# Kernel optimization log

Hardware: AMD Instinct MI355X
Metric: run time of the kernel (lower is better)

Reference implementation:

```python
import jax, jax.numpy as jnp
import numpy as np

NEG_SLOPE = 0.2
EPS = 1e-12


def setup_inputs() -> dict:
    key = jax.random.key(0)
    ks = jax.random.split(key, 12)
    N, IN, E, C, EF, NET = 100000, 512, 3200000, 16, 64, 8
    return {
        "head_feature": jax.random.normal(ks[0], (N, IN), jnp.float32),
        "tail_feature": jax.random.normal(ks[1], (N, IN), jnp.float32),
        "edge_index": jax.random.randint(ks[2], (2, E), 0, N, jnp.int32),
        "tmp_edge": jax.random.randint(ks[3], (E,), 0, NET, jnp.int32),
        "W": jax.random.normal(ks[4], (IN, C), jnp.float32) * 0.05,
        "W_e": jax.random.normal(ks[5], (EF, EF), jnp.float32) * 0.1,
        "a_l": jax.random.normal(ks[6], (1, 1, C), jnp.float32) * 0.3,
        "a_r": jax.random.normal(ks[7], (1, 1, C), jnp.float32) * 0.3,
        "a_e": jax.random.normal(ks[8], (1, 1, EF), jnp.float32) * 0.3,
        "edge_emb": jax.random.normal(ks[9], (NET, EF), jnp.float32) * 0.3,
        "res_W": jax.random.normal(ks[10], (IN, C), jnp.float32) * 0.05,
        "res_b": jax.random.normal(ks[11], (C,), jnp.float32) * 0.05,
    }


def reference(head_feature, tail_feature, W, W_e, a_l, a_r, a_e,
              edge_emb, res_W, res_b, edge_index, tmp_edge):
    N = head_feature.shape[0]
    H = a_l.shape[1]  # nhead = 1 in SimpleHGN_final's edge_GAT
    C = a_l.shape[2]
    head_ind, tail_ind = edge_index[0], edge_index[1]

    # projected node / edge-type features (dropout is identity in eval)
    h_head = (head_feature @ W).reshape(N, H, C)              # [N,H,C]
    h_tail = (tail_feature @ W).reshape(-1, H, C)             # [Nt,H,C]
    e = (edge_emb @ W_e).reshape(-1, H, a_e.shape[2])         # [NET,H,EF]

    # per-edge attention logits
    h_l = (a_l * h_head).sum(-1)[head_ind]                    # [E,H]
    h_r = (a_r * h_tail).sum(-1)[tail_ind]                    # [E,H]
    h_e = (a_e * e).sum(-1)[tmp_edge]                         # [E,H]
    logits = jax.nn.leaky_relu(h_l + h_r + h_e, NEG_SLOPE)    # [E,H]

    # sparse softmax over each destination (head) row, per head
    m = jax.ops.segment_max(logits, head_ind, num_segments=N)  # [N,H]
    ex = jnp.exp(logits - m[head_ind])
    denom = jax.ops.segment_sum(ex, head_ind, num_segments=N)  # [N,H]
    attn = ex / denom[head_ind]                                # [E,H]

    # SpMM aggregation: out[i] = sum_e attn[e] * h_tail[tail[e]]
    msg = attn[..., None] * h_tail[tail_ind]                   # [E,H,C]
    out = jax.ops.segment_sum(msg, head_ind, num_segments=N)   # [N,H,C]
    out = out.reshape(N, H * C)

    # node residual (nn.Linear on x_head)
    out = out + head_feature @ res_W + res_b

    # SimpleHGN_final post-processing: L2 row-normalize then softmax
    norm = jnp.linalg.norm(out, axis=1, keepdims=True)
    h_prime = out / jnp.maximum(norm, EPS)
    return jax.nn.softmax(h_prime, axis=1)
```

## Files before the change

### kernel.cpp

```cpp
#include <hip/hip_runtime.h>
#include <hip/hip_fp16.h>
#include <math.h>

#define IN_F 512
#define C_DIM 16
#define EF_DIM 64
#define BSHIFT 6
#define NPB 64
#define NBMAX2 2048
#define CNTW 2048
#define SCB 512
#define CAP 2560

typedef float f32x4 __attribute__((ext_vector_type(4)));
typedef unsigned u32x2 __attribute__((ext_vector_type(2)));
typedef _Float16 f16x8 __attribute__((ext_vector_type(8)));

union U2H { unsigned u; __half2 h; };

typedef const unsigned __attribute__((address_space(1)))* gas_u32;
typedef unsigned __attribute__((address_space(3)))* las_u32;

__device__ __forceinline__ void gld16(const float* g, float* l) {
  __builtin_amdgcn_global_load_lds((gas_u32)g, (las_u32)l, 16, 0, 0);
}

__global__ __launch_bounds__(512) void prep_kernel(
    const float* __restrict__ W, const float* __restrict__ We,
    const float* __restrict__ al, const float* __restrict__ ar,
    const float* __restrict__ ae, const float* __restrict__ emb,
    const float* __restrict__ resW, float* __restrict__ he,
    _Float16* __restrict__ Bph, _Float16* __restrict__ Bpt,
    float* __restrict__ wlt, float* __restrict__ wrt, int NET) {
  __shared__ float v[EF_DIM];
  int t = threadIdx.x;
  float wl = 0.f, wr = 0.f;
#pragma unroll
  for (int c = 0; c < C_DIM; c++) {
    float wv = W[t * C_DIM + c];
    wl += wv * al[c];
    wr += wv * ar[c];
  }
  wlt[t] = wl;
  wrt[t] = wr;
  if (t < EF_DIM) {
    float s = 0.f;
    for (int f = 0; f < EF_DIM; f++) s += We[t * EF_DIM + f] * ae[f];
    v[t] = s;
  }
  __syncthreads();
  if (t < NET) {
    float s = 0.f;
    for (int k = 0; k < EF_DIM; k++) s += emb[t * EF_DIM + k] * v[k];
    he[t] = s;
  }
  for (int i = 0; i < 16; i++) {
    int flat = t + 512 * i;
    int j = flat & 7;
    int l = (flat >> 3) & 63;
    int s = flat >> 9;
    int k = 32 * s + ((l >> 4) << 3) + j;
    int c = l & 15;
    Bph[flat] = (_Float16)resW[k * C_DIM + c];
    Bpt[flat] = (_Float16)W[k * C_DIM + c];
  }
}

__global__ __launch_bounds__(256) void proj7_kernel(
    const float* __restrict__ hf, const float* __restrict__ tf,
    const _Float16* __restrict__ Bph, const _Float16* __restrict__ Bpt,
    const float* __restrict__ wlt, const float* __restrict__ wrt,
    float* __restrict__ resid, float* __restrict__ hl,
    __half* __restrict__ ht_, float* __restrict__ hr, int N) {
  __shared__ float As[2][4096];
  int t = threadIdx.x;
  int w = __builtin_amdgcn_readfirstlane(t >> 6);
  int lane = t & 63;
  int r0 = blockIdx.x * 64;
  const float* feat = blockIdx.y ? tf : hf;
  const _Float16* Bp = blockIdx.y ? Bpt : Bph;
  const float* wv = blockIdx.y ? wrt : wlt;
  f32x4 acc0 = {0.f, 0.f, 0.f, 0.f};
  float acc1 = 0.f;
  const float* sg_src[4];
#pragma unroll
  for (int g = 0; g < 4; g++) {
    int u = (w * 4 + g) * 64 + lane;
    int r = u >> 4;
    int c = (u & 15) ^ (r & 7);
    int gr = min(r0 + r, N - 1);
    sg_src[g] = feat + (size_t)gr * IN_F + c * 4;
  }
  int row = w * 16 + (lane & 15);
  int sA[2][2];
#pragma unroll
  for (int s2 = 0; s2 < 2; s2++)
#pragma unroll
    for (int h = 0; h < 2; h++)
      sA[s2][h] = row * 16 + ((s2 * 8 + (lane >> 4) * 2 + h) ^ (row & 7));
  const float* wvp = wv + (lane >> 4) * 8;
#pragma unroll
  for (int g = 0; g < 4; g++) gld16(sg_src[g], &As[0][(w * 4 + g) * 256]);
  __syncthreads();
#pragma unroll
  for (int kc = 0; kc < 8; kc++) {
    if (kc < 7) {
      int nb = (kc + 1) & 1;
#pragma unroll
      for (int g = 0; g < 4; g++)
        gld16(sg_src[g] + (kc + 1) * 64, &As[nb][(w * 4 + g) * 256]);
    }
    const float* ab = As[kc & 1];
#pragma unroll
    for (int s2 = 0; s2 < 2; s2++) {
      f32x4 lo = *(const f32x4*)(ab + sA[s2][0] * 4);
      f32x4 hi = *(const f32x4*)(ab + sA[s2][1] * 4);
      f16x8 a = {(_Float16)lo.x, (_Float16)lo.y, (_Float16)lo.z,
                 (_Float16)lo.w, (_Float16)hi.x, (_Float16)hi.y,
                 (_Float16)hi.z, (_Float16)hi.w};
      int s = kc * 2 + s2;
      f16x8 b0 = *(const f16x8*)(Bp + (size_t)(s * 64 + lane) * 8);
      acc0 = __builtin_amdgcn_mfma_f32_16x16x32_f16(a, b0, acc0, 0, 0, 0);
      f32x4 wa = *(const f32x4*)(wvp + kc * 64 + s2 * 32);
      f32x4 wb = *(const f32x4*)(wvp + kc * 64 + s2 * 32 + 4);
      acc1 += lo.x * wa.x + lo.y * wa.y + lo.z * wa.z + lo.w * wa.w +
              hi.x * wb.x + hi.y * wb.y + hi.z * wb.z + hi.w * wb.w;
    }
    __syncthreads();
  }
  acc1 += __shfl_xor(acc1, 16, 64);
  acc1 += __shfl_xor(acc1, 32, 64);
  int col = lane & 15;
  int rb = r0 + w * 16 + (lane >> 4) * 4;
#pragma unroll
  for (int i = 0; i < 4; i++) {
    int r = rb + i;
    if (r < N) {
      if (blockIdx.y == 0)
        resid[(size_t)r * C_DIM + col] = acc0[i];
      else
        ht_[(size_t)r * C_DIM + col] = __float2half(acc0[i]);
    }
  }
  if (lane < 16) {
    int r = r0 + w * 16 + lane;
    if (r < N) {
      if (blockIdx.y == 0)
        hl[r] = acc1;
      else
        hr[r] = acc1;
    }
  }
}

__global__ __launch_bounds__(512) void hist_kernel(
    const int* __restrict__ head, unsigned* __restrict__ cnt, int E, int NB,
    int chunk) {
  __shared__ unsigned lcnt[NBMAX2];
  int tid = threadIdx.x;
  for (int b = tid; b < NB; b += 512) lcnt[b] = 0u;
  __syncthreads();
  int start = blockIdx.x * chunk;
  int end = min(E, start + chunk);
  for (int i = start + tid; i < end; i += 512)
    atomicAdd(&lcnt[((unsigned)__builtin_nontemporal_load(head + i)) >> BSHIFT],
              1u);
  __syncthreads();
  unsigned* row = cnt + (size_t)blockIdx.x * CNTW;
  for (int b = tid; b < NB; b += 512) row[b] = lcnt[b];
}

__global__ __launch_bounds__(256) void colscan_kernel(
    unsigned* __restrict__ cnt, unsigned* __restrict__ btotal, int NB) {
  int b = blockIdx.x * 256 + threadIdx.x;
  if (b >= NB) return;
  unsigned running = 0;
#pragma unroll 8
  for (int blk = 0; blk < SCB; blk++) {
    unsigned v = cnt[(size_t)blk * CNTW + b];
    cnt[(size_t)blk * CNTW + b] = running;
    running += v;
  }
  btotal[b] = running;
}

__global__ __launch_bounds__(1024) void scan_kernel(
    const unsigned* __restrict__ btotal, unsigned* __restrict__ base, int NB) {
  __shared__ unsigned ps[1024];
  int t = threadIdx.x;
  unsigned a = (2 * t < NB) ? btotal[2 * t] : 0u;
  unsigned b = (2 * t + 1 < NB) ? btotal[2 * t + 1] : 0u;
  ps[t] = a + b;
  __syncthreads();
  for (int off = 1; off < 1024; off <<= 1) {
    unsigned v = (t >= off) ? ps[t - off] : 0u;
    __syncthreads();
    ps[t] += v;
    __syncthreads();
  }
  unsigned excl = ps[t] - (a + b);
  if (2 * t < NB) base[2 * t] = excl;
  if (2 * t + 1 < NB) base[2 * t + 1] = excl + a;
  if (t == 1023) base[NB] = ps[1023];
}

__global__ __launch_bounds__(512) void scatter_kernel(
    const int* __restrict__ head, const int* __restrict__ tail,
    const int* __restrict__ ty, const unsigned* __restrict__ cnt,
    const unsigned* __restrict__ bbase, unsigned* __restrict__ rec, int E,
    int NB, int chunk) {
  __shared__ unsigned lbase[NBMAX2];
  __shared__ unsigned lcnt[NBMAX2];
  int tid = threadIdx.x;
  const unsigned* row = cnt + (size_t)blockIdx.x * CNTW;
  for (int b = tid; b < NB; b += 512) {
    lbase[b] = bbase[b] + row[b];
    lcnt[b] = 0u;
  }
  __syncthreads();
  int start = blockIdx.x * chunk;
  int end = min(E, start + chunk);
  for (int i = start + tid; i < end; i += 512) {
    unsigned h = (unsigned)__builtin_nontemporal_load(head + i);
    unsigned tl = (unsigned)__builtin_nontemporal_load(tail + i);
    unsigned t = (unsigned)__builtin_nontemporal_load(ty + i);
    unsigned b = h >> BSHIFT;
    unsigned off = atomicAdd(&lcnt[b], 1u);
    rec[lbase[b] + off] = ((h & 63u) << 20) | ((t & 7u) << 17) | tl;
  }
}

__global__ __launch_bounds__(256) void agg_kernel(
    const unsigned* __restrict__ rec, const unsigned* __restrict__ base,
    const __half* __restrict__ ht, const float* __restrict__ h_l,
    const float* __restrict__ h_r, const float* __restrict__ he_tab,
    const float* __restrict__ resid, const float* __restrict__ resb,
    float* __restrict__ out, int N, int NET) {
  __shared__ unsigned srec[CAP];
  __shared__ unsigned scnt[NPB];
  __shared__ unsigned soff[NPB + 1];
  __shared__ unsigned scur[NPB];
  __shared__ float accf[NPB * 18];
  __shared__ float hl_s[NPB];
  __shared__ float he_s[8];
  int tid = threadIdx.x;
  int b = blockIdx.x;
  int nodebase = b << BSHIFT;
  int s = (int)base[b];
  int e = (int)base[b + 1];
  int cnt_all = e - s;
  int m = min(cnt_all, CAP);
  if (tid < NPB) {
    scnt[tid] = 0u;
    int node = nodebase + tid;
    hl_s[tid] = node < N ? h_l[node] : 0.f;
  }
  if (tid < NET) he_s[tid] = he_tab[tid];
  for (int i = tid; i < NPB * 18; i += 256) accf[i] = 0.f;
  __syncthreads();
  for (int i = tid; i < m; i += 256)
    atomicAdd(&scnt[rec[(size_t)(s + i)] >> 20], 1u);
  __syncthreads();
  if (tid < NPB) {
    unsigned v = scnt[tid];
    unsigned orig = v;
    for (int off = 1; off < NPB; off <<= 1) {
      unsigned u = __shfl_up(v, off, 64);
      if (tid >= off) v += u;
    }
    soff[tid + 1] = v;
    scur[tid] = v - orig;
    if (tid == 0) soff[0] = 0u;
  }
  __syncthreads();
  for (int i = tid; i < m; i += 256) {
    unsigned r = rec[(size_t)(s + i)];
    unsigned pos = atomicAdd(&scur[r >> 20], 1u);
    srec[pos] = r;
  }
  for (int i = CAP + tid; i < cnt_all; i += 256) {
    unsigned r = rec[(size_t)(s + i)];
    int local = (int)(r >> 20);
    int typ = (int)((r >> 17) & 7u);
    int tl = (int)(r & 0x1FFFFu);
    float lg = hl_s[local] + h_r[tl] + he_s[typ];
    lg = lg > 0.f ? lg : 0.2f * lg;
    float ex = __expf(lg);
    const uint4* hp = (const uint4*)(ht + (size_t)tl * C_DIM);
    uint4 A = hp[0], B = hp[1];
    float* a = accf + local * 18;
    U2H cv;
    float2 f;
    unsigned wvv[8] = {A.x, A.y, A.z, A.w, B.x, B.y, B.z, B.w};
#pragma unroll
    for (int q = 0; q < 8; q++) {
      cv.u = wvv[q];
      f = __half22float2(cv.h);
      atomicAdd(a + 2 * q, ex * f.x);
      atomicAdd(a + 2 * q + 1, ex * f.y);
    }
    atomicAdd(a + 16, ex);
  }
  __syncthreads();
  int w = tid >> 6;
  int lane = tid & 63;
  int node_l = w * 16 + (lane >> 2);
  int p = lane & 3;
  float a[17];
#pragma unroll
  for (int k = 0; k < 17; k++) a[k] = 0.f;
  int st = (int)soff[node_l];
  int en = (int)soff[node_l + 1];
  float hlv = hl_s[node_l];
  for (int i = st + p; i < en; i += 4) {
    unsigned r = srec[i];
    int typ = (int)((r >> 17) & 7u);
    int tl = (int)(r & 0x1FFFFu);
    float lg = hlv + h_r[tl] + he_s[typ];
    lg = lg > 0.f ? lg : 0.2f * lg;
    float ex = __expf(lg);
    const uint4* hp = (const uint4*)(ht + (size_t)tl * C_DIM);
    uint4 A = hp[0], B = hp[1];
    U2H cv;
    float2 f;
    unsigned wd[8] = {A.x, A.y, A.z, A.w, B.x, B.y, B.z, B.w};
#pragma unroll
    for (int q = 0; q < 8; q++) {
      cv.u = wd[q];
      f = __half22float2(cv.h);
      a[2 * q] += ex * f.x;
      a[2 * q + 1] += ex * f.y;
    }
    a[16] += ex;
  }
#pragma unroll
  for (int k = 0; k < 17; k++) {
    a[k] += __shfl_xor(a[k], 1, 64);
    a[k] += __shfl_xor(a[k], 2, 64);
  }
  if (p != 0) return;
  int node = nodebase + node_l;
  if (node >= N) return;
  float d = a[16] + accf[node_l * 18 + 16];
  float inv = d > 0.f ? 1.f / d : 0.f;
  const f32x4* r4 = (const f32x4*)(resid + (size_t)node * C_DIM);
  float o[C_DIM];
  float ss = 0.f;
#pragma unroll
  for (int q = 0; q < 4; q++) {
    f32x4 rr = __builtin_nontemporal_load(r4 + q);
    o[4 * q + 0] =
        (a[4 * q + 0] + accf[node_l * 18 + 4 * q + 0]) * inv + rr.x + resb[4 * q + 0];
    o[4 * q + 1] =
        (a[4 * q + 1] + accf[node_l * 18 + 4 * q + 1]) * inv + rr.y + resb[4 * q + 1];
    o[4 * q + 2] =
        (a[4 * q + 2] + accf[node_l * 18 + 4 * q + 2]) * inv + rr.z + resb[4 * q + 2];
    o[4 * q + 3] =
        (a[4 * q + 3] + accf[node_l * 18 + 4 * q + 3]) * inv + rr.w + resb[4 * q + 3];
  }
#pragma unroll
  for (int cc = 0; cc < C_DIM; cc++) ss += o[cc] * o[cc];
  float sc = 1.f / fmaxf(sqrtf(ss), 1e-12f);
  float mx = -1e30f;
#pragma unroll
  for (int cc = 0; cc < C_DIM; cc++) {
    o[cc] *= sc;
    mx = fmaxf(mx, o[cc]);
  }
  float sum = 0.f;
#pragma unroll
  for (int cc = 0; cc < C_DIM; cc++) {
    o[cc] = __expf(o[cc] - mx);
    sum += o[cc];
  }
  float isum = 1.f / sum;
  f32x4* o4 = (f32x4*)(out + (size_t)node * C_DIM);
#pragma unroll
  for (int q = 0; q < 4; q++) {
    f32x4 ov;
    ov.x = o[4 * q] * isum;
    ov.y = o[4 * q + 1] * isum;
    ov.z = o[4 * q + 2] * isum;
    ov.w = o[4 * q + 3] * isum;
    __builtin_nontemporal_store(ov, o4 + q);
  }
}

extern "C" void kernel_launch(void* const* d_in, const int* in_sizes, int n_in,
                              void* d_out, int out_size, void* d_ws,
                              size_t ws_size, hipStream_t stream) {
  const float* head_feature = (const float*)d_in[0];
  const float* tail_feature = (const float*)d_in[1];
  const int* edge_index = (const int*)d_in[2];
  const int* tmp_edge = (const int*)d_in[3];
  const float* W = (const float*)d_in[4];
  const float* We = (const float*)d_in[5];
  const float* al = (const float*)d_in[6];
  const float* ar = (const float*)d_in[7];
  const float* ae = (const float*)d_in[8];
  const float* emb = (const float*)d_in[9];
  const float* resW = (const float*)d_in[10];
  const float* resb = (const float*)d_in[11];

  const int C = in_sizes[6];
  const int IN = in_sizes[4] / C;
  const int N = in_sizes[0] / IN;
  const int E = in_sizes[3];
  const int EF = in_sizes[8];
  const int NET = in_sizes[9] / EF;
  const int NB = (N + NPB - 1) / NPB;
  (void)C; (void)IN; (void)EF; (void)ws_size; (void)out_size; (void)n_in;

  const int* head = edge_index;
  const int* tail = edge_index + E;

  float* ws = (float*)d_ws;
  float* he = ws;
  _Float16* Bph = (_Float16*)(he + 32);
  _Float16* Bpt = Bph + 8192;
  float* wlt = (float*)(Bpt + 8192);
  float* wrt = wlt + 512;
  float* h_l = wrt + 512;
  float* h_r = h_l + N;
  __half* ht = (__half*)(h_r + N);
  float* resid = (float*)(ht + (size_t)C_DIM * N);
  unsigned* rec = (unsigned*)(resid + (size_t)C_DIM * N);
  unsigned* cnt = rec + (size_t)E;
  unsigned* btotal = cnt + (size_t)SCB * CNTW;
  unsigned* bbase = btotal + NBMAX2;

  prep_kernel<<<1, 512, 0, stream>>>(W, We, al, ar, ae, emb, resW, he, Bph,
                                     Bpt, wlt, wrt, NET);
  dim3 pg((N + 63) / 64, 2);
  proj7_kernel<<<pg, 256, 0, stream>>>(head_feature, tail_feature, Bph, Bpt,
                                       wlt, wrt, resid, h_l, ht, h_r, N);

  int chunk = (E + SCB - 1) / SCB;
  hist_kernel<<<SCB, 512, 0, stream>>>(head, cnt, E, NB, chunk);
  colscan_kernel<<<(NB + 255) / 256, 256, 0, stream>>>(cnt, btotal, NB);
  scan_kernel<<<1, 1024, 0, stream>>>(btotal, bbase, NB);
  scatter_kernel<<<SCB, 512, 0, stream>>>(head, tail, tmp_edge, cnt, bbase,
                                          rec, E, NB, chunk);
  agg_kernel<<<NB, 256, 0, stream>>>(rec, bbase, ht, h_l, h_r, he, resid,
                                     resb, (float*)d_out, N, NET);
}
```

Baseline: 244.0 us.

## Fuse histogram into projection kernel and precompute edge exp in scatter

Merges the edge-head histogram pass into the projection kernel as extra blocks, so the two independent jobs share one launch and can overlap. Moves the attention-logit computation (h_l+h_r+h_e, leaky relu, exp) from the aggregation kernel into the scatter kernel, which now writes 8-byte records (packed index plus exp value). The intent is to remove the random h_r gathers and exp work from the aggregation critical path. In exchange the record buffer doubles in size, adding write and read traffic, and agg uses twice the shared memory for staged records, which may lower occupancy.

Result: slower. 270.4 us (+10.8%).

```diff
diff --git a/kernel.cpp b/kernel.cpp
--- a/kernel.cpp
+++ b/kernel.cpp
@@ -66,20 +66,42 @@
   }
 }
 
-__global__ __launch_bounds__(256) void proj7_kernel(
+__global__ __launch_bounds__(256) void projhist_kernel(
     const float* __restrict__ hf, const float* __restrict__ tf,
     const _Float16* __restrict__ Bph, const _Float16* __restrict__ Bpt,
     const float* __restrict__ wlt, const float* __restrict__ wrt,
     float* __restrict__ resid, float* __restrict__ hl,
-    __half* __restrict__ ht_, float* __restrict__ hr, int N) {
-  __shared__ float As[2][4096];
+    __half* __restrict__ ht_, float* __restrict__ hr, int N, int PB,
+    const int* __restrict__ head, unsigned* __restrict__ cnt, int E, int NB,
+    int chunk) {
+  __shared__ __align__(16) float shmem[8192];
   int t = threadIdx.x;
+  int bid = blockIdx.x;
+  if (bid >= 2 * PB) {
+    unsigned* lcnt = (unsigned*)shmem;
+    int hb = bid - 2 * PB;
+    for (int b = t; b < NB; b += 256) lcnt[b] = 0u;
+    __syncthreads();
+    int start = hb * chunk;
+    int end = min(E, start + chunk);
+    for (int i = start + t; i < end; i += 256)
+      atomicAdd(
+          &lcnt[((unsigned)__builtin_nontemporal_load(head + i)) >> BSHIFT],
+          1u);
+    __syncthreads();
+    unsigned* row = cnt + (size_t)hb * CNTW;
+    for (int b = t; b < NB; b += 256) row[b] = lcnt[b];
+    return;
+  }
+  float* As0 = shmem;
+  float* As1 = shmem + 4096;
   int w = __builtin_amdgcn_readfirstlane(t >> 6);
   int lane = t & 63;
-  int r0 = blockIdx.x * 64;
-  const float* feat = blockIdx.y ? tf : hf;
-  const _Float16* Bp = blockIdx.y ? Bpt : Bph;
-  const float* wv = blockIdx.y ? wrt : wlt;
+  int by = bid >= PB ? 1 : 0;
+  int r0 = (bid - by * PB) * 64;
+  const float* feat = by ? tf : hf;
+  const _Float16* Bp = by ? Bpt : Bph;
+  const float* wv = by ? wrt : wlt;
   f32x4 acc0 = {0.f, 0.f, 0.f, 0.f};
   float acc1 = 0.f;
   const float* sg_src[4];
@@ -100,17 +122,17 @@
       sA[s2][h] = row * 16 + ((s2 * 8 + (lane >> 4) * 2 + h) ^ (row & 7));
   const float* wvp = wv + (lane >> 4) * 8;
 #pragma unroll
-  for (int g = 0; g < 4; g++) gld16(sg_src[g], &As[0][(w * 4 + g) * 256]);
+  for (int g = 0; g < 4; g++) gld16(sg_src[g], As0 + (w * 4 + g) * 256);
   __syncthreads();
 #pragma unroll
   for (int kc = 0; kc < 8; kc++) {
     if (kc < 7) {
-      int nb = (kc + 1) & 1;
+      float* nb = (kc & 1) ? As0 : As1;
 #pragma unroll
       for (int g = 0; g < 4; g++)
-        gld16(sg_src[g] + (kc + 1) * 64, &As[nb][(w * 4 + g) * 256]);
-    }
-    const float* ab = As[kc & 1];
+        gld16(sg_src[g] + (kc + 1) * 64, nb + (w * 4 + g) * 256);
+    }
+    const float* ab = (kc & 1) ? As1 : As0;
 #pragma unroll
     for (int s2 = 0; s2 < 2; s2++) {
       f32x4 lo = *(const f32x4*)(ab + sA[s2][0] * 4);
@@ -136,7 +158,7 @@
   for (int i = 0; i < 4; i++) {
     int r = rb + i;
     if (r < N) {
-      if (blockIdx.y == 0)
+      if (by == 0)
         resid[(size_t)r * C_DIM + col] = acc0[i];
       else
         ht_[(size_t)r * C_DIM + col] = __float2half(acc0[i]);
@@ -145,29 +167,12 @@
   if (lane < 16) {
     int r = r0 + w * 16 + lane;
     if (r < N) {
-      if (blockIdx.y == 0)
+      if (by == 0)
         hl[r] = acc1;
       else
         hr[r] = acc1;
     }
   }
-}
-
-__global__ __launch_bounds__(512) void hist_kernel(
-    const int* __restrict__ head, unsigned* __restrict__ cnt, int E, int NB,
-    int chunk) {
-  __shared__ unsigned lcnt[NBMAX2];
-  int tid = threadIdx.x;
-  for (int b = tid; b < NB; b += 512) lcnt[b] = 0u;
-  __syncthreads();
-  int start = blockIdx.x * chunk;
-  int end = min(E, start + chunk);
-  for (int i = start + tid; i < end; i += 512)
-    atomicAdd(&lcnt[((unsigned)__builtin_nontemporal_load(head + i)) >> BSHIFT],
-              1u);
-  __syncthreads();
-  unsigned* row = cnt + (size_t)blockIdx.x * CNTW;
-  for (int b = tid; b < NB; b += 512) row[b] = lcnt[b];
 }
 
 __global__ __launch_bounds__(256) void colscan_kernel(
@@ -206,12 +211,15 @@
 
 __global__ __launch_bounds__(512) void scatter_kernel(
     const int* __restrict__ head, const int* __restrict__ tail,
-    const int* __restrict__ ty, const unsigned* __restrict__ cnt,
-    const unsigned* __restrict__ bbase, unsigned* __restrict__ rec, int E,
-    int NB, int chunk) {
+    const int* __restrict__ ty, const float* __restrict__ h_l,
+    const float* __restrict__ h_r, const float* __restrict__ he_tab,
+    const unsigned* __restrict__ cnt, const unsigned* __restrict__ bbase,
+    unsigned* __restrict__ rec, int E, int NB, int chunk, int NET) {
   __shared__ unsigned lbase[NBMAX2];
   __shared__ unsigned lcnt[NBMAX2];
+  __shared__ float he_s[32];
   int tid = threadIdx.x;
+  if (tid < NET) he_s[tid] = he_tab[tid];
   const unsigned* row = cnt + (size_t)blockIdx.x * CNTW;
   for (int b = tid; b < NB; b += 512) {
     lbase[b] = bbase[b] + row[b];
@@ -222,44 +230,41 @@
   int end = min(E, start + chunk);
   for (int i = start + tid; i < end; i += 512) {
     unsigned h = (unsigned)__builtin_nontemporal_load(head + i);
-    unsigned tl = (unsigned)__builtin_nontemporal_load(tail + i);
-    unsigned t = (unsigned)__builtin_nontemporal_load(ty + i);
+    int tl = __builtin_nontemporal_load(tail + i);
+    int t = __builtin_nontemporal_load(ty + i);
+    float lg = h_l[h] + h_r[tl] + he_s[t];
+    lg = lg > 0.f ? lg : 0.2f * lg;
+    float ex = __expf(lg);
     unsigned b = h >> BSHIFT;
     unsigned off = atomicAdd(&lcnt[b], 1u);
-    rec[lbase[b] + off] = ((h & 63u) << 20) | ((t & 7u) << 17) | tl;
+    u32x2* dst = (u32x2*)(rec + 2 * (size_t)(lbase[b] + off));
+    u32x2 rv;
+    rv.x = ((h & 63u) << 17) | (unsigned)tl;
+    rv.y = __float_as_uint(ex);
+    *dst = rv;
   }
 }
 
 __global__ __launch_bounds__(256) void agg_kernel(
     const unsigned* __restrict__ rec, const unsigned* __restrict__ base,
-    const __half* __restrict__ ht, const float* __restrict__ h_l,
-    const float* __restrict__ h_r, const float* __restrict__ he_tab,
-    const float* __restrict__ resid, const float* __restrict__ resb,
-    float* __restrict__ out, int N, int NET) {
-  __shared__ unsigned srec[CAP];
+    const __half* __restrict__ ht, const float* __restrict__ resid,
+    const float* __restrict__ resb, float* __restrict__ out, int N) {
+  __shared__ __align__(16) unsigned srec[CAP * 2];
   __shared__ unsigned scnt[NPB];
   __shared__ unsigned soff[NPB + 1];
   __shared__ unsigned scur[NPB];
   __shared__ float accf[NPB * 18];
-  __shared__ float hl_s[NPB];
-  __shared__ float he_s[8];
   int tid = threadIdx.x;
   int b = blockIdx.x;
-  int nodebase = b << BSHIFT;
   int s = (int)base[b];
   int e = (int)base[b + 1];
   int cnt_all = e - s;
   int m = min(cnt_all, CAP);
-  if (tid < NPB) {
-    scnt[tid] = 0u;
-    int node = nodebase + tid;
-    hl_s[tid] = node < N ? h_l[node] : 0.f;
-  }
-  if (tid < NET) he_s[tid] = he_tab[tid];
+  if (tid < NPB) scnt[tid] = 0u;
   for (int i = tid; i < NPB * 18; i += 256) accf[i] = 0.f;
   __syncthreads();
   for (int i = tid; i < m; i += 256)
-    atomicAdd(&scnt[rec[(size_t)(s + i)] >> 20], 1u);
+    atomicAdd(&scnt[rec[2 * (size_t)(s + i)] >> 17], 1u);
   __syncthreads();
   if (tid < NPB) {
     unsigned v = scnt[tid];
@@ -274,18 +279,15 @@
   }
   __syncthreads();
   for (int i = tid; i < m; i += 256) {
-    unsigned r = rec[(size_t)(s + i)];
-    unsigned pos = atomicAdd(&scur[r >> 20], 1u);
-    srec[pos] = r;
+    u32x2 r = *(const u32x2*)(rec + 2 * (size_t)(s + i));
+    unsigned pos = atomicAdd(&scur[r.x >> 17], 1u);
+    *(u32x2*)(srec + 2 * pos) = r;
   }
   for (int i = CAP + tid; i < cnt_all; i += 256) {
-    unsigned r = rec[(size_t)(s + i)];
-    int local = (int)(r >> 20);
-    int typ = (int)((r >> 17) & 7u);
-    int tl = (int)(r & 0x1FFFFu);
-    float lg = hl_s[local] + h_r[tl] + he_s[typ];
-    lg = lg > 0.f ? lg : 0.2f * lg;
-    float ex = __expf(lg);
+    u32x2 r = *(const u32x2*)(rec + 2 * (size_t)(s + i));
+    int local = (int)(r.x >> 17);
+    int tl = (int)(r.x & 0x1FFFFu);
+    float ex = __uint_as_float(r.y);
     const uint4* hp = (const uint4*)(ht + (size_t)tl * C_DIM);
     uint4 A = hp[0], B = hp[1];
     float* a = accf + local * 18;
@@ -311,14 +313,10 @@
   for (int k = 0; k < 17; k++) a[k] = 0.f;
   int st = (int)soff[node_l];
   int en = (int)soff[node_l + 1];
-  float hlv = hl_s[node_l];
   for (int i = st + p; i < en; i += 4) {
-    unsigned r = srec[i];
-    int typ = (int)((r >> 17) & 7u);
-    int tl = (int)(r & 0x1FFFFu);
-    float lg = hlv + h_r[tl] + he_s[typ];
-    lg = lg > 0.f ? lg : 0.2f * lg;
-    float ex = __expf(lg);
+    u32x2 r = *(const u32x2*)(srec + 2 * (size_t)i);
+    int tl = (int)(r.x & 0x1FFFFu);
+    float ex = __uint_as_float(r.y);
     const uint4* hp = (const uint4*)(ht + (size_t)tl * C_DIM);
     uint4 A = hp[0], B = hp[1];
     U2H cv;
@@ -339,7 +337,7 @@
     a[k] += __shfl_xor(a[k], 2, 64);
   }
   if (p != 0) return;
-  int node = nodebase + node_l;
+  int node = (b << BSHIFT) + node_l;
   if (node >= N) return;
   float d = a[16] + accf[node_l * 18 + 16];
   float inv = d > 0.f ? 1.f / d : 0.f;
@@ -425,22 +423,21 @@
   __half* ht = (__half*)(h_r + N);
   float* resid = (float*)(ht + (size_t)C_DIM * N);
   unsigned* rec = (unsigned*)(resid + (size_t)C_DIM * N);
-  unsigned* cnt = rec + (size_t)E;
+  unsigned* cnt = rec + 2 * (size_t)E;
   unsigned* btotal = cnt + (size_t)SCB * CNTW;
   unsigned* bbase = btotal + NBMAX2;
 
   prep_kernel<<<1, 512, 0, stream>>>(W, We, al, ar, ae, emb, resW, he, Bph,
                                      Bpt, wlt, wrt, NET);
-  dim3 pg((N + 63) / 64, 2);
-  proj7_kernel<<<pg, 256, 0, stream>>>(head_feature, tail_feature, Bph, Bpt,
-                                       wlt, wrt, resid, h_l, ht, h_r, N);
-
+  int PB = (N + 63) / 64;
   int chunk = (E + SCB - 1) / SCB;
-  hist_kernel<<<SCB, 512, 0, stream>>>(head, cnt, E, NB, chunk);
+  projhist_kernel<<<2 * PB + SCB, 256, 0, stream>>>(
+      head_feature, tail_feature, Bph, Bpt, wlt, wrt, resid, h_l, ht, h_r, N,
+      PB, head, cnt, E, NB, chunk);
   colscan_kernel<<<(NB + 255) / 256, 256, 0, stream>>>(cnt, btotal, NB);
   scan_kernel<<<1, 1024, 0, stream>>>(btotal, bbase, NB);
-  scatter_kernel<<<SCB, 512, 0, stream>>>(head, tail, tmp_edge, cnt, bbase,
-                                          rec, E, NB, chunk);
-  agg_kernel<<<NB, 256, 0, stream>>>(rec, bbase, ht, h_l, h_r, he, resid,
-                                     resb, (float*)d_out, N, NET);
-}
+  scatter_kernel<<<SCB, 512, 0, stream>>>(head, tail, tmp_edge, h_l, h_r, he,
+                                          cnt, bbase, rec, E, NB, chunk, NET);
+  agg_kernel<<<NB, 256, 0, stream>>>(rec, bbase, ht, resid, resb,
+                                     (float*)d_out, N);
+}
```
